# Performance work log

Hardware: AMD Instinct MI355X
Metric: run time of the kernel (lower is better)

## Reference

```python
import jax, jax.numpy as jnp
import numpy as np

B, I, H, T = 256, 256, 512, 400


def setup_inputs() -> dict:
    key = jax.random.key(0)
    k1, k2, k3, k4, k5 = jax.random.split(key, 5)
    s = 1.0 / np.sqrt(H)  # PyTorch LSTMCell init scale (values only matter for realism)
    return {
        "x": jax.random.normal(k1, (B, I, T), dtype=jnp.float32),
        "w_ih": jax.random.normal(k2, (4 * H, I), dtype=jnp.float32) * s,
        "w_hh": jax.random.normal(k3, (4 * H, H), dtype=jnp.float32) * s,
        "b_ih": jax.random.normal(k4, (4 * H,), dtype=jnp.float32) * s,
        "b_hh": jax.random.normal(k5, (4 * H,), dtype=jnp.float32) * s,
    }


def reference(x, w_ih, w_hh, b_ih, b_hh):
    # x: [B, I, T] -> time-major [T, B, I]
    x_t = jnp.transpose(x, (2, 0, 1))
    # Precompute input-side gate contributions (batched GEMM, parallel over T)
    xg = jnp.einsum("tbi,gi->tbg", x_t, w_ih) + b_ih + b_hh  # [T, B, 4H]

    h0 = jnp.zeros((x.shape[0], w_hh.shape[1]), dtype=x.dtype)
    c0 = jnp.zeros_like(h0)

    def step(carry, xg_t):
        h, c = carry
        gates = xg_t + h @ w_hh.T  # [B, 4H]
        i, f, g, o = jnp.split(gates, 4, axis=-1)  # PyTorch gate order i,f,g,o
        i = jax.nn.sigmoid(i)
        f = jax.nn.sigmoid(f)
        g = jnp.tanh(g)
        o = jax.nn.sigmoid(o)
        c_new = f * c + i * g
        h_new = o * jnp.tanh(c_new)
        return (h_new, c_new), c_new

    (h_T, c_T), c_stack = jax.lax.scan(step, (h0, c0), xg)
    return c_stack  # [T, B, H] -- the per-step cell states the module stores
```

## Files before the change

### kernel.cpp

```cpp
#include <hip/hip_runtime.h>
#include <stdint.h>

#define TT 400
#define BB 256
#define II 256
#define HH 512
#define NG 2048

typedef __attribute__((ext_vector_type(8))) _Float16 half8;
typedef __attribute__((ext_vector_type(4))) float f32x4;
typedef __attribute__((ext_vector_type(4))) unsigned int u32x4;
typedef unsigned int u32;
typedef unsigned short u16;

static __device__ __forceinline__ u32 f2hbits(float f){
  union { _Float16 h; u16 u; } c; c.h = (_Float16)f; return (u32)c.u;
}

#define GLOAD16(gsrc, ldst) \
  __builtin_amdgcn_global_load_lds((const __attribute__((address_space(1))) void*)(gsrc), \
                                   (__attribute__((address_space(3))) void*)(ldst), 16, 0, 0)

__global__ __launch_bounds__(256) void k_prep_x(const float* __restrict__ x,
                                                u16* __restrict__ xT){
  __shared__ float tile[32][17];
  const int bid = blockIdx.x;
  const int tb = bid % 25, ib = (bid / 25) & 7, b = bid / 200;
  const int t0 = tb * 16, i0 = ib * 32;
  const int tl = threadIdx.x & 15, il = threadIdx.x >> 4;
  tile[il][tl]      = x[(size_t)(b * II + i0 + il) * TT + t0 + tl];
  tile[il + 16][tl] = x[(size_t)(b * II + i0 + il + 16) * TT + t0 + tl];
  __syncthreads();
  const int t_l = threadIdx.x >> 4, ip = threadIdx.x & 15;
  const u32 pack = f2hbits(tile[2 * ip][t_l]) | (f2hbits(tile[2 * ip + 1][t_l]) << 16);
  *(u32*)(xT + ((size_t)(t0 + t_l) * BB + b) * II + i0 + 2 * ip) = pack;
}

__global__ __launch_bounds__(256) void k_prep_w(const float* __restrict__ w_ih,
                                                u16* __restrict__ Wp){
  const size_t idx = (size_t)blockIdx.x * 256 + threadIdx.x;
  const float4 v = *(const float4*)(w_ih + idx * 4);
  uint2 o;
  o.x = f2hbits(v.x) | (f2hbits(v.y) << 16);
  o.y = f2hbits(v.z) | (f2hbits(v.w) << 16);
  *(uint2*)(Wp + idx * 4) = o;
}

__global__ __launch_bounds__(256) void k_gemm_xg(const u16* __restrict__ A,
                                                 const u16* __restrict__ B,
                                                 _Float16* __restrict__ xg){
  __shared__ char lds[65536];
  const int tid = threadIdx.x, w = tid >> 6, lane = tid & 63;
  const int nb = blockIdx.x & 15, mb = blockIdx.x >> 4;
  const size_t m0 = (size_t)mb * 128;
  const int n0 = nb * 128;
  const int lr = lane & 15, lh = lane >> 4;

  auto stage = [&](int it, int buf){
    const size_t kb = (size_t)it * 128;
    #pragma unroll
    for (int i2 = 0; i2 < 4; ++i2){
      const int u = w * 256 + i2 * 64 + lane;
      const int r = u >> 3, s = u & 7;
      const char* g = (const char*)A + (m0 + r) * 512 + kb + ((s ^ (r & 7)) << 4);
      char* l = lds + buf * 16384 + ((w * 256 + i2 * 64) << 4);
      GLOAD16(g, l);
    }
    #pragma unroll
    for (int i2 = 0; i2 < 4; ++i2){
      const int u = w * 256 + i2 * 64 + lane;
      const int r = u >> 3, s = u & 7;
      const char* g = (const char*)B + (size_t)(n0 + r) * 512 + kb + ((s ^ (r & 7)) << 4);
      char* l = lds + 32768 + buf * 16384 + ((w * 256 + i2 * 64) << 4);
      GLOAD16(g, l);
    }
  };

  f32x4 acc[4][4];
  #pragma unroll
  for (int i = 0; i < 4; ++i)
    #pragma unroll
    for (int j = 0; j < 4; ++j){ f32x4 z = {0.f,0.f,0.f,0.f}; acc[i][j] = z; }

  const int wm = (w & 1) * 64, wn = (w >> 1) * 64;
  stage(0, 0);
  for (int it = 0; it < 4; ++it){
    const int buf = it & 1;
    if (it < 3) stage(it + 1, buf ^ 1);
    __syncthreads();
    const char* lA = lds + buf * 16384;
    const char* lB = lds + 32768 + buf * 16384;
    #pragma unroll
    for (int ks = 0; ks < 2; ++ks){
      half8 a[4], b[4];
      const int s = ks * 4 + lh;
      #pragma unroll
      for (int mt = 0; mt < 4; ++mt){
        const int r = wm + mt * 16 + lr;
        a[mt] = *(const half8*)(lA + r * 128 + ((s ^ (r & 7)) << 4));
      }
      #pragma unroll
      for (int nt = 0; nt < 4; ++nt){
        const int r = wn + nt * 16 + lr;
        b[nt] = *(const half8*)(lB + r * 128 + ((s ^ (r & 7)) << 4));
      }
      #pragma unroll
      for (int mt = 0; mt < 4; ++mt)
        #pragma unroll
        for (int nt = 0; nt < 4; ++nt)
          acc[mt][nt] = __builtin_amdgcn_mfma_f32_16x16x32_f16(a[mt], b[nt], acc[mt][nt], 0, 0, 0);
    }
    __syncthreads();
  }
  #pragma unroll
  for (int mt = 0; mt < 4; ++mt)
    #pragma unroll
    for (int nt = 0; nt < 4; ++nt)
      #pragma unroll
      for (int r = 0; r < 4; ++r){
        const size_t row = m0 + wm + mt * 16 + lh * 4 + r;
        const int col = n0 + wn + nt * 16 + lr;
        xg[row * NG + col] = (_Float16)acc[mt][nt][r];
      }
}

__global__ __launch_bounds__(512) void k_lstm(const _Float16* __restrict__ xg,
    const float* __restrict__ w_hh, const float* __restrict__ b_ih,
    const float* __restrict__ b_hh, u32* __restrict__ htag,
    float* __restrict__ out){
  extern __shared__ char lds[];
  char* Wl = lds;
  char* hb = lds + 131072;
  float* gbuf = (float*)(lds + 147456);

  const int tid = threadIdx.x, w = tid >> 6, lane = tid & 63;
  const int lr = lane & 15, lh = lane >> 4;
  const int gb = blockIdx.x >> 4, gn = blockIdx.x & 15;
  const int b0 = gb * 16, j0 = gn * 32;

  for (int rep = 0; rep < 16; ++rep){
    const int u = rep * 512 + tid;
    const int row = u >> 6, u0 = u & 63;
    const int grow = ((row >> 5) << 9) + j0 + (row & 31);
    const float* src = w_hh + (size_t)grow * HH + u0 * 8;
    const float4 va = *(const float4*)src;
    const float4 vb = *(const float4*)(src + 4);
    union { _Float16 h[8]; u32x4 v; } p;
    p.h[0] = (_Float16)va.x; p.h[1] = (_Float16)va.y;
    p.h[2] = (_Float16)va.z; p.h[3] = (_Float16)va.w;
    p.h[4] = (_Float16)vb.x; p.h[5] = (_Float16)vb.y;
    p.h[6] = (_Float16)vb.z; p.h[7] = (_Float16)vb.w;
    *(u32x4*)(Wl + row * 1024 + ((u0 ^ (row & 7)) << 4)) = p.v;
  }
  const int brow = tid >> 5;
  const int jj   = tid & 31;
  float bias_[4];
  #pragma unroll
  for (int q = 0; q < 4; ++q) bias_[q] = b_ih[q * HH + j0 + jj] + b_hh[q * HH + j0 + jj];
  float c = 0.f;
  const int q = w >> 1, jb = w & 1;

  const int u1 = tid, u2 = tid + 512;
  const int r1 = u1 >> 6, c1 = u1 & 63;
  const int r2 = u2 >> 6, c2 = u2 & 63;
  const size_t gof1 = (size_t)(b0 + r1) * 512 + c1 * 8;
  const size_t gof2 = (size_t)(b0 + r2) * 512 + c2 * 8;
  const int lof1 = r1 * 1024 + ((c1 ^ (r1 & 7)) << 4);
  const int lof2 = r2 * 1024 + ((c2 ^ (r2 & 7)) << 4);
  u32* pst0 = htag + (size_t)(b0 + brow) * 512 + (j0 + jj);
  __syncthreads();

  for (int t = 0; t < TT; ++t){
    const _Float16* xt = xg + (size_t)t * (BB * NG) + (size_t)(b0 + brow) * NG + j0 + jj;
    u32 xv0, xv1, xv2, xv3;
    asm volatile(
      "global_load_ushort %0, %4, off\n\t"
      "global_load_ushort %1, %5, off\n\t"
      "global_load_ushort %2, %6, off\n\t"
      "global_load_ushort %3, %7, off"
      : "=&v"(xv0), "=&v"(xv1), "=&v"(xv2), "=&v"(xv3)
      : "v"(xt), "v"(xt + HH), "v"(xt + 2 * HH), "v"(xt + 3 * HH)
      : "memory");

    if (t > 0){
      const u32* gbase = htag + (size_t)((t - 1) & 1) * 131072;
      const u32* g1 = gbase + gof1;
      const u32* g2 = gbase + gof2;
      const u32 te = ((u32)t) << 16;
      u32x4 a0, a1, d0, d1;
      int need = 3, guard = 0;
      do {
        if (need & 1)
          asm volatile("global_load_dwordx4 %0, %2, off sc0 sc1\n\t"
                       "global_load_dwordx4 %1, %3, off sc0 sc1"
                       : "=&v"(a0), "=&v"(a1) : "v"(g1), "v"(g1 + 4) : "memory");
        if (need & 2)
          asm volatile("global_load_dwordx4 %0, %2, off sc0 sc1\n\t"
                       "global_load_dwordx4 %1, %3, off sc0 sc1"
                       : "=&v"(d0), "=&v"(d1) : "v"(g2), "v"(g2 + 4) : "memory");
        asm volatile("s_waitcnt vmcnt(0)" ::: "memory");
        if (need & 1){
          u32 m = (a0[0]^te)|(a0[1]^te)|(a0[2]^te)|(a0[3]^te)
                 |(a1[0]^te)|(a1[1]^te)|(a1[2]^te)|(a1[3]^te);
          if (!(m >> 16)) need &= ~1;
        }
        if (need & 2){
          u32 m = (d0[0]^te)|(d0[1]^te)|(d0[2]^te)|(d0[3]^te)
                 |(d1[0]^te)|(d1[1]^te)|(d1[2]^te)|(d1[3]^te);
          if (!(m >> 16)) need &= ~2;
        }
      } while (need && ++guard < (1 << 18));
      u32x4 p1, p2;
      p1[0] = (a0[0] & 0xffffu) | (a0[1] << 16);
      p1[1] = (a0[2] & 0xffffu) | (a0[3] << 16);
      p1[2] = (a1[0] & 0xffffu) | (a1[1] << 16);
      p1[3] = (a1[2] & 0xffffu) | (a1[3] << 16);
      p2[0] = (d0[0] & 0xffffu) | (d0[1] << 16);
      p2[1] = (d0[2] & 0xffffu) | (d0[3] << 16);
      p2[2] = (d1[0] & 0xffffu) | (d1[1] << 16);
      p2[3] = (d1[2] & 0xffffu) | (d1[3] << 16);
      *(u32x4*)(hb + lof1) = p1;
      *(u32x4*)(hb + lof2) = p2;
      __syncthreads();
      f32x4 ac0 = {0.f,0.f,0.f,0.f}, ac1 = {0.f,0.f,0.f,0.f};
      const int nrow = q * 32 + jb * 16 + lr;
      const int nbase = nrow * 1024, nx = nrow & 7, ax = lr & 7;
      const char* abase = hb + lr * 1024;
      #pragma unroll
      for (int ks = 0; ks < 16; ks += 2){
        const int s0 = ks * 4 + lh, s1 = s0 + 4;
        const half8 av0 = *(const half8*)(abase + ((s0 ^ ax) << 4));
        const half8 bv0 = *(const half8*)(Wl + nbase + ((s0 ^ nx) << 4));
        ac0 = __builtin_amdgcn_mfma_f32_16x16x32_f16(av0, bv0, ac0, 0, 0, 0);
        const half8 av1 = *(const half8*)(abase + ((s1 ^ ax) << 4));
        const half8 bv1 = *(const half8*)(Wl + nbase + ((s1 ^ nx) << 4));
        ac1 = __builtin_amdgcn_mfma_f32_16x16x32_f16(av1, bv1, ac1, 0, 0, 0);
      }
      const f32x4 acs = ac0 + ac1;
      #pragma unroll
      for (int r = 0; r < 4; ++r)
        gbuf[(q * 16 + lh * 4 + r) * 32 + jb * 16 + lr] = acs[r];
      __syncthreads();
    }
    asm volatile("s_waitcnt vmcnt(0)" ::: "memory");
    asm volatile("" : "+v"(xv0), "+v"(xv1), "+v"(xv2), "+v"(xv3));

    float g4[4];
    {
      union { u32 u; _Float16 h[2]; } cv;
      cv.u = xv0; g4[0] = (float)cv.h[0] + bias_[0];
      cv.u = xv1; g4[1] = (float)cv.h[0] + bias_[1];
      cv.u = xv2; g4[2] = (float)cv.h[0] + bias_[2];
      cv.u = xv3; g4[3] = (float)cv.h[0] + bias_[3];
    }
    if (t > 0){
      #pragma unroll
      for (int qq = 0; qq < 4; ++qq) g4[qq] += gbuf[(qq * 16 + brow) * 32 + jj];
    }
    const float i_ = 1.f / (1.f + __expf(-g4[0]));
    const float f_ = 1.f / (1.f + __expf(-g4[1]));
    const float ea = __expf(-2.f * fabsf(g4[2]));
    const float g_ = __builtin_copysignf((1.f - ea) / (1.f + ea), g4[2]);
    const float o_ = 1.f / (1.f + __expf(-g4[3]));
    c = f_ * c + i_ * g_;
    const float eb = __expf(-2.f * fabsf(c));
    const float th = __builtin_copysignf((1.f - eb) / (1.f + eb), c);
    const float hn = o_ * th;

    if (t < TT - 1){
      u32* ph = pst0 + (size_t)(t & 1) * 131072;
      const u32 hv = f2hbits(hn) | ((u32)(t + 1) << 16);
      asm volatile("global_store_dword %0, %1, off sc0 sc1"
                   :: "v"(ph), "v"(hv) : "memory");
    }
    out[(size_t)t * (BB * HH) + (size_t)(b0 + brow) * HH + j0 + jj] = c;
  }
}

extern "C" void kernel_launch(void* const* d_in, const int* in_sizes, int n_in,
                              void* d_out, int out_size, void* d_ws, size_t ws_size,
                              hipStream_t stream){
  const float* x    = (const float*)d_in[0];
  const float* w_ih = (const float*)d_in[1];
  const float* w_hh = (const float*)d_in[2];
  const float* b_ih = (const float*)d_in[3];
  const float* b_hh = (const float*)d_in[4];
  float* out = (float*)d_out;
  char* ws = (char*)d_ws;

  const size_t o_xg  = 0;
  const size_t o_xt  = 419430400;
  const size_t o_wp  = 471859200;
  const size_t o_h   = 472907776;
  const size_t need  = 473956352;
  if (ws_size < need) return;

  _Float16* xg = (_Float16*)(ws + o_xg);
  u16* xt  = (u16*)(ws + o_xt);
  u16* wp  = (u16*)(ws + o_wp);
  u32* ht  = (u32*)(ws + o_h);

  hipLaunchKernelGGL(k_prep_x, dim3(51200), dim3(256), 0, stream, x, xt);
  hipLaunchKernelGGL(k_prep_w, dim3(512), dim3(256), 0, stream, w_ih, wp);
  hipLaunchKernelGGL(k_gemm_xg, dim3(12800), dim3(256), 0, stream, xt, wp, xg);
  hipLaunchKernelGGL(k_lstm, dim3(256), dim3(512), 155648, stream,
                     xg, w_hh, b_ih, b_hh, ht, out);
}
```

Baseline: 1.817 ms.

## Prefetch next-step xg and h-tag loads, unroll LSTM recurrence by two

```diff
diff --git a/kernel.cpp b/kernel.cpp
--- a/kernel.cpp
+++ b/kernel.cpp
@@ -135,8 +135,8 @@
 
   const int tid = threadIdx.x, w = tid >> 6, lane = tid & 63;
   const int lr = lane & 15, lh = lane >> 4;
-  const int gb = blockIdx.x >> 4, gn = blockIdx.x & 15;
-  const int b0 = gb * 16, j0 = gn * 32;
+  const int g = blockIdx.x & 15, n = blockIdx.x >> 4;
+  const int b0 = g * 16, j0 = n * 32;
 
   for (int rep = 0; rep < 16; ++rep){
     const int u = rep * 512 + tid;
@@ -154,9 +154,10 @@
   }
   const int brow = tid >> 5;
   const int jj   = tid & 31;
-  float bias_[4];
+  float biasv[4];
   #pragma unroll
-  for (int q = 0; q < 4; ++q) bias_[q] = b_ih[q * HH + j0 + jj] + b_hh[q * HH + j0 + jj];
+  for (int q2 = 0; q2 < 4; ++q2)
+    biasv[q2] = b_ih[q2 * HH + j0 + jj] + b_hh[q2 * HH + j0 + jj];
   float c = 0.f;
   const int q = w >> 1, jb = w & 1;
 
@@ -168,113 +169,151 @@
   const int lof1 = r1 * 1024 + ((c1 ^ (r1 & 7)) << 4);
   const int lof2 = r2 * 1024 + ((c2 ^ (r2 & 7)) << 4);
   u32* pst0 = htag + (size_t)(b0 + brow) * 512 + (j0 + jj);
+  const _Float16* xbase = xg + (size_t)(b0 + brow) * NG + j0 + jj;
+
+  u32x4 a0 = {0,0,0,0}, a1 = a0, d0 = a0, d1 = a0;
+
   __syncthreads();
 
-  for (int t = 0; t < TT; ++t){
-    const _Float16* xt = xg + (size_t)t * (BB * NG) + (size_t)(b0 + brow) * NG + j0 + jj;
-    u32 xv0, xv1, xv2, xv3;
-    asm volatile(
-      "global_load_ushort %0, %4, off\n\t"
-      "global_load_ushort %1, %5, off\n\t"
-      "global_load_ushort %2, %6, off\n\t"
-      "global_load_ushort %3, %7, off"
-      : "=&v"(xv0), "=&v"(xv1), "=&v"(xv2), "=&v"(xv3)
-      : "v"(xt), "v"(xt + HH), "v"(xt + 2 * HH), "v"(xt + 3 * HH)
-      : "memory");
-
-    if (t > 0){
-      const u32* gbase = htag + (size_t)((t - 1) & 1) * 131072;
-      const u32* g1 = gbase + gof1;
-      const u32* g2 = gbase + gof2;
-      const u32 te = ((u32)t) << 16;
-      u32x4 a0, a1, d0, d1;
-      int need = 3, guard = 0;
-      do {
-        if (need & 1)
-          asm volatile("global_load_dwordx4 %0, %2, off sc0 sc1\n\t"
-                       "global_load_dwordx4 %1, %3, off sc0 sc1"
-                       : "=&v"(a0), "=&v"(a1) : "v"(g1), "v"(g1 + 4) : "memory");
-        if (need & 2)
-          asm volatile("global_load_dwordx4 %0, %2, off sc0 sc1\n\t"
-                       "global_load_dwordx4 %1, %3, off sc0 sc1"
-                       : "=&v"(d0), "=&v"(d1) : "v"(g2), "v"(g2 + 4) : "memory");
-        asm volatile("s_waitcnt vmcnt(0)" ::: "memory");
-        if (need & 1){
-          u32 m = (a0[0]^te)|(a0[1]^te)|(a0[2]^te)|(a0[3]^te)
-                 |(a1[0]^te)|(a1[1]^te)|(a1[2]^te)|(a1[3]^te);
-          if (!(m >> 16)) need &= ~1;
-        }
-        if (need & 2){
-          u32 m = (d0[0]^te)|(d0[1]^te)|(d0[2]^te)|(d0[3]^te)
-                 |(d1[0]^te)|(d1[1]^te)|(d1[2]^te)|(d1[3]^te);
-          if (!(m >> 16)) need &= ~2;
-        }
-      } while (need && ++guard < (1 << 18));
-      u32x4 p1, p2;
-      p1[0] = (a0[0] & 0xffffu) | (a0[1] << 16);
-      p1[1] = (a0[2] & 0xffffu) | (a0[3] << 16);
-      p1[2] = (a1[0] & 0xffffu) | (a1[1] << 16);
-      p1[3] = (a1[2] & 0xffffu) | (a1[3] << 16);
-      p2[0] = (d0[0] & 0xffffu) | (d0[1] << 16);
-      p2[1] = (d0[2] & 0xffffu) | (d0[3] << 16);
-      p2[2] = (d1[0] & 0xffffu) | (d1[1] << 16);
-      p2[3] = (d1[2] & 0xffffu) | (d1[3] << 16);
-      *(u32x4*)(hb + lof1) = p1;
-      *(u32x4*)(hb + lof2) = p2;
-      __syncthreads();
-      f32x4 ac0 = {0.f,0.f,0.f,0.f}, ac1 = {0.f,0.f,0.f,0.f};
-      const int nrow = q * 32 + jb * 16 + lr;
-      const int nbase = nrow * 1024, nx = nrow & 7, ax = lr & 7;
-      const char* abase = hb + lr * 1024;
-      #pragma unroll
-      for (int ks = 0; ks < 16; ks += 2){
-        const int s0 = ks * 4 + lh, s1 = s0 + 4;
-        const half8 av0 = *(const half8*)(abase + ((s0 ^ ax) << 4));
-        const half8 bv0 = *(const half8*)(Wl + nbase + ((s0 ^ nx) << 4));
-        ac0 = __builtin_amdgcn_mfma_f32_16x16x32_f16(av0, bv0, ac0, 0, 0, 0);
-        const half8 av1 = *(const half8*)(abase + ((s1 ^ ax) << 4));
-        const half8 bv1 = *(const half8*)(Wl + nbase + ((s1 ^ nx) << 4));
-        ac1 = __builtin_amdgcn_mfma_f32_16x16x32_f16(av1, bv1, ac1, 0, 0, 0);
-      }
-      const f32x4 acs = ac0 + ac1;
-      #pragma unroll
-      for (int r = 0; r < 4; ++r)
-        gbuf[(q * 16 + lh * 4 + r) * 32 + jb * 16 + lr] = acs[r];
-      __syncthreads();
-    }
-    asm volatile("s_waitcnt vmcnt(0)" ::: "memory");
-    asm volatile("" : "+v"(xv0), "+v"(xv1), "+v"(xv2), "+v"(xv3));
-
-    float g4[4];
-    {
-      union { u32 u; _Float16 h[2]; } cv;
-      cv.u = xv0; g4[0] = (float)cv.h[0] + bias_[0];
-      cv.u = xv1; g4[1] = (float)cv.h[0] + bias_[1];
-      cv.u = xv2; g4[2] = (float)cv.h[0] + bias_[2];
-      cv.u = xv3; g4[3] = (float)cv.h[0] + bias_[3];
-    }
-    if (t > 0){
-      #pragma unroll
-      for (int qq = 0; qq < 4; ++qq) g4[qq] += gbuf[(qq * 16 + brow) * 32 + jj];
-    }
-    const float i_ = 1.f / (1.f + __expf(-g4[0]));
-    const float f_ = 1.f / (1.f + __expf(-g4[1]));
-    const float ea = __expf(-2.f * fabsf(g4[2]));
-    const float g_ = __builtin_copysignf((1.f - ea) / (1.f + ea), g4[2]);
-    const float o_ = 1.f / (1.f + __expf(-g4[3]));
-    c = f_ * c + i_ * g_;
-    const float eb = __expf(-2.f * fabsf(c));
-    const float th = __builtin_copysignf((1.f - eb) / (1.f + eb), c);
-    const float hn = o_ * th;
-
-    if (t < TT - 1){
-      u32* ph = pst0 + (size_t)(t & 1) * 131072;
-      const u32 hv = f2hbits(hn) | ((u32)(t + 1) << 16);
-      asm volatile("global_store_dword %0, %1, off sc0 sc1"
-                   :: "v"(ph), "v"(hv) : "memory");
-    }
-    out[(size_t)t * (BB * HH) + (size_t)(b0 + brow) * HH + j0 + jj] = c;
+  u32 xa0, xa1, xa2, xa3, xb0, xb1, xb2, xb3;
+  asm volatile(
+    "global_load_ushort %0, %4, off\n\t"
+    "global_load_ushort %1, %5, off\n\t"
+    "global_load_ushort %2, %6, off\n\t"
+    "global_load_ushort %3, %7, off"
+    : "=&v"(xa0), "=&v"(xa1), "=&v"(xa2), "=&v"(xa3)
+    : "v"(xbase), "v"(xbase + HH), "v"(xbase + 2 * HH), "v"(xbase + 3 * HH)
+    : "memory");
+
+#define STEP_BODY(T, XC0, XC1, XC2, XC3, XN0, XN1, XN2, XN3) do { \
+  if ((T) > 0){ \
+    const u32 te = ((u32)(T)) << 16; \
+    const u32* gbase = htag + (size_t)(((T) - 1) & 1) * 131072; \
+    const u32* g1 = gbase + gof1; \
+    const u32* g2 = gbase + gof2; \
+     \
+    int pend = 3, guard = 0; \
+    do { \
+      asm volatile("s_waitcnt vmcnt(0)" ::: "memory"); \
+      __builtin_amdgcn_sched_barrier(0); \
+      if (pend & 1){ \
+        const u32 m_ = (a0[0]^te)|(a0[1]^te)|(a0[2]^te)|(a0[3]^te) \
+                      |(a1[0]^te)|(a1[1]^te)|(a1[2]^te)|(a1[3]^te); \
+        if (!(m_ >> 16)){ \
+          u32x4 p1; \
+          p1[0] = (a0[0] & 0xffffu) | (a0[1] << 16); \
+          p1[1] = (a0[2] & 0xffffu) | (a0[3] << 16); \
+          p1[2] = (a1[0] & 0xffffu) | (a1[1] << 16); \
+          p1[3] = (a1[2] & 0xffffu) | (a1[3] << 16); \
+          *(u32x4*)(hb + lof1) = p1; \
+          pend &= ~1; \
+        } else { \
+          asm volatile("global_load_dwordx4 %0, %2, off sc0 sc1\n\t" \
+                       "global_load_dwordx4 %1, %3, off sc0 sc1" \
+                       : "=&v"(a0), "=&v"(a1) : "v"(g1), "v"(g1 + 4) : "memory"); \
+        } \
+      } \
+      if (pend & 2){ \
+        const u32 m_ = (d0[0]^te)|(d0[1]^te)|(d0[2]^te)|(d0[3]^te) \
+                      |(d1[0]^te)|(d1[1]^te)|(d1[2]^te)|(d1[3]^te); \
+        if (!(m_ >> 16)){ \
+          u32x4 p2; \
+          p2[0] = (d0[0] & 0xffffu) | (d0[1] << 16); \
+          p2[1] = (d0[2] & 0xffffu) | (d0[3] << 16); \
+          p2[2] = (d1[0] & 0xffffu) | (d1[1] << 16); \
+          p2[3] = (d1[2] & 0xffffu) | (d1[3] << 16); \
+          *(u32x4*)(hb + lof2) = p2; \
+          pend &= ~2; \
+        } else { \
+          asm volatile("global_load_dwordx4 %0, %2, off sc0 sc1\n\t" \
+                       "global_load_dwordx4 %1, %3, off sc0 sc1" \
+                       : "=&v"(d0), "=&v"(d1) : "v"(g2), "v"(g2 + 4) : "memory"); \
+        } \
+      } \
+    } while (pend && ++guard < (1 << 16)); \
+  } \
+   \
+  if ((T) < TT - 1){ \
+    const _Float16* xt_ = xbase + (size_t)((T) + 1) * (BB * NG); \
+    asm volatile( \
+      "global_load_ushort %0, %4, off\n\t" \
+      "global_load_ushort %1, %5, off\n\t" \
+      "global_load_ushort %2, %6, off\n\t" \
+      "global_load_ushort %3, %7, off" \
+      : "=&v"(XN0), "=&v"(XN1), "=&v"(XN2), "=&v"(XN3) \
+      : "v"(xt_), "v"(xt_ + HH), "v"(xt_ + 2 * HH), "v"(xt_ + 3 * HH) \
+      : "memory"); \
+  } \
+  float g4[4]; \
+  if ((T) > 0){ \
+    __syncthreads();                          \
+    f32x4 ac0 = {0.f,0.f,0.f,0.f}, ac1 = {0.f,0.f,0.f,0.f}; \
+    const int nrow = q * 32 + jb * 16 + lr; \
+    const int nbase = nrow * 1024, nx = nrow & 7, ax = lr & 7; \
+    const char* abase = hb + lr * 1024; \
+    _Pragma("unroll") \
+    for (int ks = 0; ks < 16; ks += 2){ \
+      const int s0 = ks * 4 + lh, s1 = s0 + 4; \
+      const half8 av0 = *(const half8*)(abase + ((s0 ^ ax) << 4)); \
+      const half8 bv0 = *(const half8*)(Wl + nbase + ((s0 ^ nx) << 4)); \
+      ac0 = __builtin_amdgcn_mfma_f32_16x16x32_f16(av0, bv0, ac0, 0, 0, 0); \
+      const half8 av1 = *(const half8*)(abase + ((s1 ^ ax) << 4)); \
+      const half8 bv1 = *(const half8*)(Wl + nbase + ((s1 ^ nx) << 4)); \
+      ac1 = __builtin_amdgcn_mfma_f32_16x16x32_f16(av1, bv1, ac1, 0, 0, 0); \
+    } \
+    const f32x4 acs = ac0 + ac1; \
+    _Pragma("unroll") \
+    for (int r = 0; r < 4; ++r) \
+      gbuf[(q * 16 + lh * 4 + r) * 32 + jb * 16 + lr] = acs[r]; \
+    __syncthreads();                          \
+  } \
+  if ((T) == 0) asm volatile("s_waitcnt vmcnt(0)" ::: "memory"); \
+  asm volatile("" : "+v"(XC0), "+v"(XC1), "+v"(XC2), "+v"(XC3)); \
+  { \
+    union { u32 u; _Float16 h[2]; } cv; \
+    cv.u = XC0; g4[0] = (float)cv.h[0] + biasv[0]; \
+    cv.u = XC1; g4[1] = (float)cv.h[0] + biasv[1]; \
+    cv.u = XC2; g4[2] = (float)cv.h[0] + biasv[2]; \
+    cv.u = XC3; g4[3] = (float)cv.h[0] + biasv[3]; \
+  } \
+  if ((T) > 0){ \
+    _Pragma("unroll") \
+    for (int qq = 0; qq < 4; ++qq) g4[qq] += gbuf[(qq * 16 + brow) * 32 + jj]; \
+  } \
+  const float i_ = 1.f / (1.f + __expf(-g4[0])); \
+  const float f_ = 1.f / (1.f + __expf(-g4[1])); \
+  const float ea = __expf(-2.f * fabsf(g4[2])); \
+  const float g_ = __builtin_copysignf((1.f - ea) / (1.f + ea), g4[2]); \
+  const float o_ = 1.f / (1.f + __expf(-g4[3])); \
+  c = f_ * c + i_ * g_; \
+  const float eb = __expf(-2.f * fabsf(c)); \
+  const float th = __builtin_copysignf((1.f - eb) / (1.f + eb), c); \
+  const float hn = o_ * th; \
+  if ((T) < TT - 1){ \
+     \
+    u32* ph = pst0 + (size_t)((T) & 1) * 131072; \
+    const u32 hv = f2hbits(hn) | ((u32)((T) + 1) << 16); \
+    asm volatile("global_store_dword %0, %1, off sc0 sc1" \
+                 :: "v"(ph), "v"(hv) : "memory"); \
+     \
+    const u32* gb_ = htag + (size_t)((T) & 1) * 131072; \
+    asm volatile( \
+      "global_load_dwordx4 %0, %4, off sc0 sc1\n\t" \
+      "global_load_dwordx4 %1, %5, off sc0 sc1\n\t" \
+      "global_load_dwordx4 %2, %6, off sc0 sc1\n\t" \
+      "global_load_dwordx4 %3, %7, off sc0 sc1" \
+      : "=&v"(a0), "=&v"(a1), "=&v"(d0), "=&v"(d1) \
+      : "v"(gb_ + gof1), "v"(gb_ + gof1 + 4), "v"(gb_ + gof2), "v"(gb_ + gof2 + 4) \
+      : "memory"); \
+  } \
+  out[(size_t)(T) * (BB * HH) + (size_t)(b0 + brow) * HH + j0 + jj] = c; \
+} while (0)
+
+  for (int t2 = 0; t2 < TT; t2 += 2){
+    STEP_BODY(t2,     xa0, xa1, xa2, xa3, xb0, xb1, xb2, xb3);
+    STEP_BODY(t2 + 1, xb0, xb1, xb2, xb3, xa0, xa1, xa2, xa3);
   }
+#undef STEP_BODY
 }
 
 extern "C" void kernel_launch(void* const* d_in, const int* in_sizes, int n_in,
@@ -300,6 +339,7 @@
   u16* wp  = (u16*)(ws + o_wp);
   u32* ht  = (u32*)(ws + o_h);
 
+  hipMemsetAsync(ht, 0, 1048576, stream);
   hipLaunchKernelGGL(k_prep_x, dim3(51200), dim3(256), 0, stream, x, xt);
   hipLaunchKernelGGL(k_prep_w, dim3(512), dim3(256), 0, stream, w_ih, wp);
   hipLaunchKernelGGL(k_gemm_xg, dim3(12800), dim3(256), 0, stream, xt, wp, xg);
```

After: 2.362 ms. 30.0% more time.

## Issue h-tag polls before x loads and overlap spin checks with LDS writes

Applied to the files above, without the earlier changes.

```diff
diff --git a/kernel.cpp b/kernel.cpp
--- a/kernel.cpp
+++ b/kernel.cpp
@@ -20,6 +20,8 @@
 #define GLOAD16(gsrc, ldst) \
   __builtin_amdgcn_global_load_lds((const __attribute__((address_space(1))) void*)(gsrc), \
                                    (__attribute__((address_space(3))) void*)(ldst), 16, 0, 0)
+
+#define BAR_LGKM() asm volatile("s_waitcnt lgkmcnt(0)\n\ts_barrier" ::: "memory")
 
 __global__ __launch_bounds__(256) void k_prep_x(const float* __restrict__ x,
                                                 u16* __restrict__ xT){
@@ -135,8 +137,8 @@
 
   const int tid = threadIdx.x, w = tid >> 6, lane = tid & 63;
   const int lr = lane & 15, lh = lane >> 4;
-  const int gb = blockIdx.x >> 4, gn = blockIdx.x & 15;
-  const int b0 = gb * 16, j0 = gn * 32;
+  const int g = blockIdx.x & 15, n = blockIdx.x >> 4;
+  const int b0 = g * 16, j0 = n * 32;
 
   for (int rep = 0; rep < 16; ++rep){
     const int u = rep * 512 + tid;
@@ -154,9 +156,10 @@
   }
   const int brow = tid >> 5;
   const int jj   = tid & 31;
-  float bias_[4];
+  float biasv[4];
   #pragma unroll
-  for (int q = 0; q < 4; ++q) bias_[q] = b_ih[q * HH + j0 + jj] + b_hh[q * HH + j0 + jj];
+  for (int q2 = 0; q2 < 4; ++q2)
+    biasv[q2] = b_ih[q2 * HH + j0 + jj] + b_hh[q2 * HH + j0 + jj];
   float c = 0.f;
   const int q = w >> 1, jb = w & 1;
 
@@ -168,10 +171,26 @@
   const int lof1 = r1 * 1024 + ((c1 ^ (r1 & 7)) << 4);
   const int lof2 = r2 * 1024 + ((c2 ^ (r2 & 7)) << 4);
   u32* pst0 = htag + (size_t)(b0 + brow) * 512 + (j0 + jj);
+  const _Float16* xbase = xg + (size_t)(b0 + brow) * NG + j0 + jj;
+
   __syncthreads();
 
   for (int t = 0; t < TT; ++t){
-    const _Float16* xt = xg + (size_t)t * (BB * NG) + (size_t)(b0 + brow) * NG + j0 + jj;
+    u32x4 a0, a1, d0, d1;
+    const u32* g1 = nullptr; const u32* g2 = nullptr;
+    if (t > 0){
+      const u32* gbase = htag + (size_t)((t - 1) & 1) * 131072;
+      g1 = gbase + gof1;
+      g2 = gbase + gof2;
+      asm volatile(
+        "global_load_dwordx4 %0, %4, off sc0 sc1\n\t"
+        "global_load_dwordx4 %1, %5, off sc0 sc1\n\t"
+        "global_load_dwordx4 %2, %6, off sc0 sc1\n\t"
+        "global_load_dwordx4 %3, %7, off sc0 sc1"
+        : "=&v"(a0), "=&v"(a1), "=&v"(d0), "=&v"(d1)
+        : "v"(g1), "v"(g1 + 4), "v"(g2), "v"(g2 + 4) : "memory");
+    }
+    const _Float16* xt = xbase + (size_t)t * (BB * NG);
     u32 xv0, xv1, xv2, xv3;
     asm volatile(
       "global_load_ushort %0, %4, off\n\t"
@@ -183,45 +202,50 @@
       : "memory");
 
     if (t > 0){
-      const u32* gbase = htag + (size_t)((t - 1) & 1) * 131072;
-      const u32* g1 = gbase + gof1;
-      const u32* g2 = gbase + gof2;
       const u32 te = ((u32)t) << 16;
-      u32x4 a0, a1, d0, d1;
-      int need = 3, guard = 0;
-      do {
-        if (need & 1)
-          asm volatile("global_load_dwordx4 %0, %2, off sc0 sc1\n\t"
-                       "global_load_dwordx4 %1, %3, off sc0 sc1"
-                       : "=&v"(a0), "=&v"(a1) : "v"(g1), "v"(g1 + 4) : "memory");
-        if (need & 2)
-          asm volatile("global_load_dwordx4 %0, %2, off sc0 sc1\n\t"
-                       "global_load_dwordx4 %1, %3, off sc0 sc1"
-                       : "=&v"(d0), "=&v"(d1) : "v"(g2), "v"(g2 + 4) : "memory");
+      asm volatile("s_waitcnt vmcnt(4)" ::: "memory");
+      __builtin_amdgcn_sched_barrier(0);
+      int pend = 3, guard = 0;
+      while (true){
+        if (pend & 1){
+          const u32 m_ = (a0[0]^te)|(a0[1]^te)|(a0[2]^te)|(a0[3]^te)
+                        |(a1[0]^te)|(a1[1]^te)|(a1[2]^te)|(a1[3]^te);
+          if (!(m_ >> 16)){
+            u32x4 p1;
+            p1[0] = (a0[0] & 0xffffu) | (a0[1] << 16);
+            p1[1] = (a0[2] & 0xffffu) | (a0[3] << 16);
+            p1[2] = (a1[0] & 0xffffu) | (a1[1] << 16);
+            p1[3] = (a1[2] & 0xffffu) | (a1[3] << 16);
+            *(u32x4*)(hb + lof1) = p1;
+            pend &= ~1;
+          } else {
+            asm volatile("global_load_dwordx4 %0, %2, off sc0 sc1\n\t"
+                         "global_load_dwordx4 %1, %3, off sc0 sc1"
+                         : "=&v"(a0), "=&v"(a1) : "v"(g1), "v"(g1 + 4) : "memory");
+          }
+        }
+        if (pend & 2){
+          const u32 m_ = (d0[0]^te)|(d0[1]^te)|(d0[2]^te)|(d0[3]^te)
+                        |(d1[0]^te)|(d1[1]^te)|(d1[2]^te)|(d1[3]^te);
+          if (!(m_ >> 16)){
+            u32x4 p2;
+            p2[0] = (d0[0] & 0xffffu) | (d0[1] << 16);
+            p2[1] = (d0[2] & 0xffffu) | (d0[3] << 16);
+            p2[2] = (d1[0] & 0xffffu) | (d1[1] << 16);
+            p2[3] = (d1[2] & 0xffffu) | (d1[3] << 16);
+            *(u32x4*)(hb + lof2) = p2;
+            pend &= ~2;
+          } else {
+            asm volatile("global_load_dwordx4 %0, %2, off sc0 sc1\n\t"
+                         "global_load_dwordx4 %1, %3, off sc0 sc1"
+                         : "=&v"(d0), "=&v"(d1) : "v"(g2), "v"(g2 + 4) : "memory");
+          }
+        }
+        if (!pend || ++guard >= (1 << 16)) break;
         asm volatile("s_waitcnt vmcnt(0)" ::: "memory");
-        if (need & 1){
-          u32 m = (a0[0]^te)|(a0[1]^te)|(a0[2]^te)|(a0[3]^te)
-                 |(a1[0]^te)|(a1[1]^te)|(a1[2]^te)|(a1[3]^te);
-          if (!(m >> 16)) need &= ~1;
-        }
-        if (need & 2){
-          u32 m = (d0[0]^te)|(d0[1]^te)|(d0[2]^te)|(d0[3]^te)
-                 |(d1[0]^te)|(d1[1]^te)|(d1[2]^te)|(d1[3]^te);
-          if (!(m >> 16)) need &= ~2;
-        }
-      } while (need && ++guard < (1 << 18));
-      u32x4 p1, p2;
-      p1[0] = (a0[0] & 0xffffu) | (a0[1] << 16);
-      p1[1] = (a0[2] & 0xffffu) | (a0[3] << 16);
-      p1[2] = (a1[0] & 0xffffu) | (a1[1] << 16);
-      p1[3] = (a1[2] & 0xffffu) | (a1[3] << 16);
-      p2[0] = (d0[0] & 0xffffu) | (d0[1] << 16);
-      p2[1] = (d0[2] & 0xffffu) | (d0[3] << 16);
-      p2[2] = (d1[0] & 0xffffu) | (d1[1] << 16);
-      p2[3] = (d1[2] & 0xffffu) | (d1[3] << 16);
-      *(u32x4*)(hb + lof1) = p1;
-      *(u32x4*)(hb + lof2) = p2;
-      __syncthreads();
+        __builtin_amdgcn_sched_barrier(0);
+      }
+      BAR_LGKM();
       f32x4 ac0 = {0.f,0.f,0.f,0.f}, ac1 = {0.f,0.f,0.f,0.f};
       const int nrow = q * 32 + jb * 16 + lr;
       const int nbase = nrow * 1024, nx = nrow & 7, ax = lr & 7;
@@ -240,7 +264,7 @@
       #pragma unroll
       for (int r = 0; r < 4; ++r)
         gbuf[(q * 16 + lh * 4 + r) * 32 + jb * 16 + lr] = acs[r];
-      __syncthreads();
+      BAR_LGKM();
     }
     asm volatile("s_waitcnt vmcnt(0)" ::: "memory");
     asm volatile("" : "+v"(xv0), "+v"(xv1), "+v"(xv2), "+v"(xv3));
@@ -248,10 +272,10 @@
     float g4[4];
     {
       union { u32 u; _Float16 h[2]; } cv;
-      cv.u = xv0; g4[0] = (float)cv.h[0] + bias_[0];
-      cv.u = xv1; g4[1] = (float)cv.h[0] + bias_[1];
-      cv.u = xv2; g4[2] = (float)cv.h[0] + bias_[2];
-      cv.u = xv3; g4[3] = (float)cv.h[0] + bias_[3];
+      cv.u = xv0; g4[0] = (float)cv.h[0] + biasv[0];
+      cv.u = xv1; g4[1] = (float)cv.h[0] + biasv[1];
+      cv.u = xv2; g4[2] = (float)cv.h[0] + biasv[2];
+      cv.u = xv3; g4[3] = (float)cv.h[0] + biasv[3];
     }
     if (t > 0){
       #pragma unroll
@@ -300,6 +324,7 @@
   u16* wp  = (u16*)(ws + o_wp);
   u32* ht  = (u32*)(ws + o_h);
 
+  hipMemsetAsync(ht, 0, 1048576, stream);
   hipLaunchKernelGGL(k_prep_x, dim3(51200), dim3(256), 0, stream, x, xt);
   hipLaunchKernelGGL(k_prep_w, dim3(512), dim3(256), 0, stream, w_ih, wp);
   hipLaunchKernelGGL(k_gemm_xg, dim3(12800), dim3(256), 0, stream, xt, wp, xg);
```

Result: slower. 2.165 ms (+19.2%).
